# Optimization experiments

Measured on AMD Instinct MI355X. Metric: run time of the kernel, lower is better.

The kernel has to match this reference:

```python
import jax, jax.numpy as jnp
import numpy as np

# Dimensions
NT, NS = 1000, 2048   # timesteps, basins
NF, NG = 6, 32        # forcing channels, static attributes
NH, NR, HS = 16, 8, 256  # buckets, routing taps, hidden size
NK, NGD = 3, 9        # len(kDict)=3 (km,ki,ke), len(gDict)=9


def setup_inputs() -> dict:
    key = jax.random.key(0)
    ks = jax.random.split(key, 16)
    # Physically plausible forcings: Prcp/Evp nonnegative, T1<=T2 (min/max temp)
    Prcp = jax.random.uniform(ks[0], (NT, NS)) * 10.0
    Evp = jax.random.uniform(ks[1], (NT, NS)) * 5.0
    Tm = jax.random.normal(ks[2], (NT, NS)) * 10.0
    T1 = Tm - jax.random.uniform(ks[3], (NT, NS)) * 5.0
    T2 = Tm + jax.random.uniform(ks[4], (NT, NS)) * 5.0
    Rad = jax.random.uniform(ks[5], (NT, NS))
    Hum = jax.random.uniform(ks[6], (NT, NS))
    x = jnp.stack([Prcp, Evp, T1, T2, Rad, Hum], axis=-1)  # [nt, ns, 6]
    xc = jax.random.normal(ks[7], (NS, NG))

    def lin(k, fan_in, fan_out, s=0.05):
        k1, k2 = jax.random.split(k)
        return (jax.random.normal(k1, (fan_in, fan_out)) * s,
                jax.random.normal(k2, (fan_out,)) * s)

    W_fc, b_fc = lin(ks[8], NG, HS)
    W_r, b_r = lin(ks[9], HS, NH * (NR + 1))
    W_g, b_g = lin(ks[10], HS, NH * NGD)
    W_kin, b_kin = lin(ks[11], 4, HS)
    W_kout, b_kout = lin(ks[12], HS, NH * NK)
    return dict(x=x, xc=xc, W_fc=W_fc, b_fc=b_fc, W_r=W_r, b_r=b_r,
                W_g=W_g, b_g=b_g, W_kin=W_kin, b_kin=b_kin,
                W_kout=W_kout, b_kout=b_kout)


def _hardsigmoid(v):
    return jnp.clip(v / 6.0 + 0.5, 0.0, 1.0)


def _forward(x, xc, W_fc, b_fc, W_r, b_r, W_g, b_g, W_kin, b_kin, W_kout, b_kout):
    nt, ns, _ = x.shape
    Prcp, Evp, T1, T2 = x[..., 0], x[..., 1], x[..., 2], x[..., 3]
    f = x[..., 2:]                        # [nt, ns, 4] (T1,T2,Rad,Hum)

    # ---- getParam (eval mode: DropMask is identity) ----
    state = xc @ W_fc + b_fc              # [ns, hs]
    pK = jnp.tanh(f @ W_kin + b_kin + state) @ W_kout + b_kout  # [nt, ns, nh*3]
    hG = jnp.tanh(state)
    pG = hG @ W_g + b_g                   # [ns, nh*9]
    pR = hG @ W_r + b_r                   # [ns, nh*(nr+1)]

    # sepParam(K): km=exp, ki=relu, ke=exp  -> time-varying [nt, ns, nh]
    km = jnp.exp(pK[..., 0 * NH:1 * NH])
    ki = jax.nn.relu(pK[..., 1 * NH:2 * NH])
    ke = jnp.exp(pK[..., 2 * NH:3 * NH])

    # sepParam(G): static [ns, nh]
    g = lambda i: pG[..., i * NH:(i + 1) * NH]
    kp = jax.nn.sigmoid(g(0))
    ks_ = jax.nn.sigmoid(g(1))
    kd = jax.nn.sigmoid(g(2))
    gd = jax.nn.sigmoid(g(3))
    gl = (jax.nn.sigmoid(g(4)) * 10.0) ** 3
    qb = jax.nn.relu(g(5)) / 10.0
    ga = jax.nn.softmax(g(6), axis=-1)    # area weights over buckets
    gi = _hardsigmoid(g(7)) / 2.0
    ge = jax.nn.relu(g(8))

    # onePeakWeight: unimodal routing weights [ns, nh, nr]
    r = pR.reshape(ns, NH, NR + 1)
    s = jax.nn.softmax(r, axis=-1)
    c = jnp.cumsum(s, axis=-1)
    w = jnp.minimum(c, 1.0 - c + s)[..., :NR]
    wr = w / jnp.sum(w, axis=-1, keepdims=True)

    # divideP: snow/liquid split from min/max temperature crossing 0 C
    fl = jnp.clip(T2 / (T2 - T1 + 1e-5), 0.0, 1.0)  # liquid fraction
    Pl = (Prcp * fl)[..., None]           # [nt, ns, 1]
    Ps = (Prcp * (1.0 - fl))[..., None]
    Ev = Evp[..., None]

    # ---- bucket.step recurrence over time (the custom-scan hot loop) ----
    def step(carry, inp):
        Sf, Ss, Sg = carry                # each [ns, nh]
        Ps_t, Pl_t, Ev_t, km_t, ki_t, ke_t = inp
        # snow bucket: accumulate, melt capped by degree-day factor km
        Sf = Sf + Ps_t
        qf = jnp.minimum(Sf, km_t)
        Sf = Sf - qf
        # partition inflow: impervious/direct fraction gi
        inflow = qf + Pl_t
        qd = inflow * gi
        Ss = Ss + inflow * (1.0 - gi)
        # evapotranspiration
        E = jnp.minimum(jnp.maximum(Ss, 0.0), Ev_t * ke_t * ge)
        Ss = Ss - E
        # interflow capped by ki
        qi = jnp.minimum(ki_t, jnp.maximum(Ss, 0.0))
        Ss = Ss - qi
        # quick flow above capacity gl, slow drainage below
        qp = kp * jnp.maximum(Ss - gl, 0.0)
        qsa = ks_ * jnp.clip(Ss, 0.0, gl)
        Ss = Ss - qp - qsa
        # deep/groundwater bucket: fraction gd percolates, linear reservoir kd + baseflow qb
        Sg = Sg + qsa * gd
        qg = kd * Sg + qb
        Sg = Sg * (1.0 - kd)
        q = qp + qsa * (1.0 - gd) + qg + qd + qi
        return (Sf, Ss, Sg), q

    init = (jnp.zeros((ns, NH), x.dtype),
            jnp.zeros((ns, NH), x.dtype),
            jnp.zeros((ns, NH), x.dtype))
    _, Qp = jax.lax.scan(step, init, (Ps, Pl, Ev, km, ki, ke))  # [nt, ns, nh]

    # routing: valid temporal convolution with per-bucket unit hydrograph wr
    Tout = nt - NR + 1
    Q = jnp.zeros((Tout, ns, NH), Qp.dtype)
    for rr in range(NR):  # NR is a small fixed constant
        Q = Q + Qp[NR - 1 - rr: nt - rr] * wr[..., rr]
    yOut = jnp.sum(Q * ga, axis=-1)       # [Tout, ns]
    return yOut


def reference(x, xc, W_fc, b_fc, W_r, b_r, W_g, b_g, W_kin, b_kin, W_kout, b_kout):
    return _forward(x, xc, W_fc, b_fc, W_r, b_r, W_g, b_g, W_kin, b_kin, W_kout, b_kout)
```

## Files before the change

kernel.cpp:

```cpp
#include <hip/hip_runtime.h>
#include <hip/hip_bf16.h>

#define NT   1000
#define NS   2048
#define NH   16
#define NR   8
#define HS   256
#define TOUT 993

typedef __attribute__((ext_vector_type(8))) short short8;
typedef __attribute__((ext_vector_type(4))) float f32x4;

__device__ __forceinline__ ushort f2bf(float f) {
    union { float f; unsigned int u; } v; v.f = f;
    unsigned int u = v.u;
    return (ushort)((u + 0x7fffu + ((u >> 16) & 1u)) >> 16);
}
__device__ __forceinline__ float bf2f(ushort u) {
    union { unsigned int i; float f; } v; v.i = ((unsigned int)u) << 16; return v.f;
}
__device__ __forceinline__ unsigned int packbf2(float lo, float hi) {
    union { __hip_bfloat162 b; unsigned int u; } v;
    v.b = __float22bfloat162_rn(make_float2(lo, hi));
    return v.u;
}
__device__ __forceinline__ float sigf(float x) { return 1.f / (1.f + __expf(-x)); }
__device__ __forceinline__ float fast_tanh(float z) {
    float e = exp2f(z * 2.885390082f);
    return 1.f - 2.f * __builtin_amdgcn_rcpf(e + 1.f);
}
__device__ __forceinline__ float2 f2fma(float s, float2 w, float2 acc) {
    return make_float2(fmaf(s, w.x, acc.x), fmaf(s, w.y, acc.y));
}
template<int CTRL>
__device__ __forceinline__ float dpp_add(float v) {
    int s = __builtin_amdgcn_update_dpp(0, __builtin_bit_cast(int, v), CTRL, 0xf, 0xf, true);
    return v + __builtin_bit_cast(float, s);
}

__global__ __launch_bounds__(256) void kA(
    const float* __restrict__ xc, const float* __restrict__ W_fc, const float* __restrict__ b_fc,
    const float* __restrict__ W_r, const float* __restrict__ b_r,
    const float* __restrict__ W_g, const float* __restrict__ b_g,
    const float* __restrict__ b_kin, const float* __restrict__ W_kout,
    float* __restrict__ stateK, float* __restrict__ params, ushort* __restrict__ Wt_g)
{
    __shared__ float xcs[32];
    __shared__ float hG[256];
    __shared__ float pGR[288];
    const int s = blockIdx.x, tid = threadIdx.x;

    if (tid < 32) xcs[tid] = xc[s * 32 + tid];
    __syncthreads();

    float acc = b_fc[tid];
#pragma unroll 8
    for (int k = 0; k < 32; ++k) acc = fmaf(xcs[k], W_fc[k * 256 + tid], acc);
    stateK[s * 256 + tid] = acc + b_kin[tid];
    hG[tid] = tanhf(acc);
    __syncthreads();

    for (int j = tid; j < 288; j += 256) {
        const float* W = (j < 144) ? W_g : W_r;
        const float* b = (j < 144) ? b_g : b_r;
        int col = (j < 144) ? j : (j - 144);
        float a = b[col];
#pragma unroll 4
        for (int k = 0; k < 256; ++k) a = fmaf(hG[k], W[k * 144 + col], a);
        pGR[j] = a;
    }
    __syncthreads();

    if (tid < 16) {
        const int h = tid;
        float g0 = pGR[h],       g1 = pGR[16 + h],  g2 = pGR[32 + h];
        float g3 = pGR[48 + h],  g4 = pGR[64 + h],  g5 = pGR[80 + h];
        float g6 = pGR[96 + h],  g7 = pGR[112 + h], g8 = pGR[128 + h];
        float kp = sigf(g0), ksg = sigf(g1), kd = sigf(g2), gd = sigf(g3);
        float t4 = sigf(g4) * 10.f; float gl = t4 * t4 * t4;
        float qb = fmaxf(g5, 0.f) * 0.1f;
        float gi = fminf(fmaxf(g7 * (1.f / 6.f) + 0.5f, 0.f), 1.f) * 0.5f;
        float ge = fmaxf(g8, 0.f);
        float m = g6;
        for (int o = 1; o < 16; o <<= 1) m = fmaxf(m, __shfl_xor(m, o));
        float e = __expf(g6 - m), esum = e;
        for (int o = 1; o < 16; o <<= 1) esum += __shfl_xor(esum, o);
        float ga = e / esum;
        float r[9], rm = -1e30f;
#pragma unroll
        for (int i = 0; i < 9; ++i) { r[i] = pGR[144 + h * 9 + i]; rm = fmaxf(rm, r[i]); }
        float er[9], es = 0.f;
#pragma unroll
        for (int i = 0; i < 9; ++i) { er[i] = __expf(r[i] - rm); es += er[i]; }
        float inv_es = 1.f / es, c = 0.f, wsum = 0.f, w[8];
#pragma unroll
        for (int i = 0; i < 8; ++i) {
            float si = er[i] * inv_es; c += si;
            float wi = fminf(c, 1.f - c + si);
            w[i] = wi; wsum += wi;
        }
        const int base = s * 16 + h;
        params[0 * 32768 + base] = kp;       params[1 * 32768 + base] = ksg;
        params[2 * 32768 + base] = kd;       params[3 * 32768 + base] = gd;
        params[4 * 32768 + base] = gl;       params[5 * 32768 + base] = qb;
        params[6 * 32768 + base] = gi;       params[7 * 32768 + base] = 1.f - gi;
        params[8 * 32768 + base] = 1.f - kd; params[9 * 32768 + base] = 1.f - gd;
        params[10 * 32768 + base] = ge;
        float sc = ga / wsum;
#pragma unroll
        for (int i = 0; i < 8; ++i) params[(11 + i) * 32768 + base] = w[i] * sc;
    }

    if (s == 0) {
        for (int i = tid; i < 48 * 256; i += 256) {
            int k = i / 48, col = i - k * 48;
            Wt_g[col * 264 + k] = f2bf(W_kout[i]);
        }
    }
}

__global__ __launch_bounds__(256, 3) void kB(
    const float* __restrict__ x,
    const float* __restrict__ stateK, const float* __restrict__ W_kin, const float* __restrict__ b_kout,
    const ushort* __restrict__ Wt_g, const float* __restrict__ params,
    unsigned int* __restrict__ kmki, ushort* __restrict__ kevA,
    float2* __restrict__ pspl)
{
    __shared__ ushort Wt[48 * 264];
    __shared__ float  stS[16 * 260];
    __shared__ float  wkS[1024];
    __shared__ float  geS[256];
    __shared__ float  evS[4][5][16];
    const int tid = threadIdx.x;
    const int st = blockIdx.x & 127;
    const int tg = blockIdx.x >> 7;
    const int s0 = st << 4;

    for (int i = tid; i < 3168; i += 256)
        ((uint2*)Wt)[i] = ((const uint2*)Wt_g)[i];
#pragma unroll
    for (int i = tid; i < 1024; i += 256) {
        int row = i >> 6, c = (i & 63) << 2;
        *(float4*)(stS + row * 260 + c) = *(const float4*)(stateK + (s0 + row) * 256 + c);
    }
    *(float4*)(wkS + tid * 4) = ((const float4*)W_kin)[tid];
    geS[tid] = params[10 * 32768 + s0 * 16 + tid];
    __syncthreads();

    const int wv = tid >> 6, lane = tid & 63;
    const int mi = lane & 15, quad = lane >> 4;
    const int site = s0 + mi;
    const int t0 = tg * 20 + wv * 5;

    float xf[5][4];
#pragma unroll
    for (int ti = 0; ti < 5; ++ti) {
        const int t = t0 + ti;
        const int xb = (t * 2048 + site) * 6;
        float2 u23 = *(const float2*)(x + xb + 2);
        float2 u45 = *(const float2*)(x + xb + 4);
        xf[ti][0] = u23.x; xf[ti][1] = u23.y; xf[ti][2] = u45.x; xf[ti][3] = u45.y;
        if (lane < 16) {
            float2 u01 = *(const float2*)(x + xb);
            float fl = fminf(fmaxf(u23.y * __builtin_amdgcn_rcpf(u23.y - u23.x + 1e-5f), 0.f), 1.f);
            const int sg = st * 4 + (mi >> 2), sl = mi & 3;
            pspl[(sg * 1000 + t) * 4 + sl] = make_float2(u01.x * (1.f - fl), u01.x * fl);
            evS[wv][ti][mi] = u01.y;
        }
    }

    const float* stp = stS + mi * 260 + quad * 8;
    const float* wkp = wkS + quad * 8;
    const ushort* Wt0 = Wt + mi * 264 + quad * 8;

    f32x4 acc[5][3];
#pragma unroll
    for (int ti = 0; ti < 5; ++ti)
#pragma unroll
        for (int j = 0; j < 3; ++j) acc[ti][j] = (f32x4){0.f, 0.f, 0.f, 0.f};

#pragma unroll 1
    for (int kk = 0; kk < 8; ++kk) {
        const int ko = kk * 32;
        float4 sa  = *(const float4*)(stp + ko);
        float4 sb  = *(const float4*)(stp + ko + 4);
        float4 w0a = *(const float4*)(wkp + ko);
        float4 w0b = *(const float4*)(wkp + ko + 4);
        float4 w1a = *(const float4*)(wkp + 256 + ko);
        float4 w1b = *(const float4*)(wkp + 256 + ko + 4);
        float4 w2a = *(const float4*)(wkp + 512 + ko);
        float4 w2b = *(const float4*)(wkp + 512 + ko + 4);
        float4 w3a = *(const float4*)(wkp + 768 + ko);
        float4 w3b = *(const float4*)(wkp + 768 + ko + 4);
        short8 b0 = *(const short8*)(Wt0 + ko);
        short8 b1 = *(const short8*)(Wt0 + 16 * 264 + ko);
        short8 b2 = *(const short8*)(Wt0 + 32 * 264 + ko);
#pragma unroll
        for (int ti = 0; ti < 5; ++ti) {
            const float x0 = xf[ti][0], x1 = xf[ti][1], x2 = xf[ti][2], x3 = xf[ti][3];
            float2 z0 = make_float2(sa.x, sa.y), z1 = make_float2(sa.z, sa.w);
            float2 z2 = make_float2(sb.x, sb.y), z3 = make_float2(sb.z, sb.w);
            z0 = f2fma(x0, make_float2(w0a.x, w0a.y), z0);
            z1 = f2fma(x0, make_float2(w0a.z, w0a.w), z1);
            z2 = f2fma(x0, make_float2(w0b.x, w0b.y), z2);
            z3 = f2fma(x0, make_float2(w0b.z, w0b.w), z3);
            z0 = f2fma(x1, make_float2(w1a.x, w1a.y), z0);
            z1 = f2fma(x1, make_float2(w1a.z, w1a.w), z1);
            z2 = f2fma(x1, make_float2(w1b.x, w1b.y), z2);
            z3 = f2fma(x1, make_float2(w1b.z, w1b.w), z3);
            z0 = f2fma(x2, make_float2(w2a.x, w2a.y), z0);
            z1 = f2fma(x2, make_float2(w2a.z, w2a.w), z1);
            z2 = f2fma(x2, make_float2(w2b.x, w2b.y), z2);
            z3 = f2fma(x2, make_float2(w2b.z, w2b.w), z3);
            z0 = f2fma(x3, make_float2(w3a.x, w3a.y), z0);
            z1 = f2fma(x3, make_float2(w3a.z, w3a.w), z1);
            z2 = f2fma(x3, make_float2(w3b.x, w3b.y), z2);
            z3 = f2fma(x3, make_float2(w3b.z, w3b.w), z3);
            union { short8 s; unsigned int u[4]; } a;
            a.u[0] = packbf2(fast_tanh(z0.x), fast_tanh(z0.y));
            a.u[1] = packbf2(fast_tanh(z1.x), fast_tanh(z1.y));
            a.u[2] = packbf2(fast_tanh(z2.x), fast_tanh(z2.y));
            a.u[3] = packbf2(fast_tanh(z3.x), fast_tanh(z3.y));
            acc[ti][0] = __builtin_amdgcn_mfma_f32_16x16x32_bf16(a.s, b0, acc[ti][0], 0, 0, 0);
            acc[ti][1] = __builtin_amdgcn_mfma_f32_16x16x32_bf16(a.s, b1, acc[ti][1], 0, 0, 0);
            acc[ti][2] = __builtin_amdgcn_mfma_f32_16x16x32_bf16(a.s, b2, acc[ti][2], 0, 0, 0);
        }
    }

    const float bo0 = b_kout[mi], bo1 = b_kout[16 + mi], bo2 = b_kout[32 + mi];
    const int sgW = st * 4 + quad;
#pragma unroll
    for (int ti = 0; ti < 5; ++ti) {
        const int t = t0 + ti;
#pragma unroll
        for (int reg = 0; reg < 4; ++reg) {
            const int sl = quad * 4 + reg;
            float km = __expf(acc[ti][0][reg] + bo0);
            float ki = fmaxf(acc[ti][1][reg] + bo1, 0.f);
            float ke = __expf(acc[ti][2][reg] + bo2);
            float kev = ke * evS[wv][ti][sl] * geS[sl * 16 + mi];
            const int idx = (sgW * 1000 + t) * 64 + (reg << 4) + mi;
            kmki[idx] = (unsigned int)f2bf(km) | ((unsigned int)f2bf(ki) << 16);
            kevA[idx] = f2bf(kev);
        }
    }
}

__global__ __launch_bounds__(64, 1) void kC(
    const unsigned int* __restrict__ kmki, const ushort* __restrict__ kevA,
    const float2* __restrict__ pspl,
    const float* __restrict__ params, float* __restrict__ yOut)
{
    const int tid = threadIdx.x;
    const int sg = blockIdx.x;
    const int sl = tid >> 4;
    const int s = sg * 4 + sl;
    const int h = tid & 15;
    const int gid = s * 16 + h;

    const float kp  = params[0 * 32768 + gid];
    const float ks_ = params[1 * 32768 + gid];
    const float kd  = params[2 * 32768 + gid];
    const float gd  = params[3 * 32768 + gid];
    const float gl  = params[4 * 32768 + gid];
    const float qbv = params[5 * 32768 + gid];
    const float gi  = params[6 * 32768 + gid];
    const float gi1 = params[7 * 32768 + gid];
    const float kd1 = params[8 * 32768 + gid];
    const float gd1 = params[9 * 32768 + gid];
    float wrga[8];
#pragma unroll
    for (int i = 0; i < 8; ++i) wrga[i] = params[(11 + i) * 32768 + gid];

    float Sf = 0.f, Ss = 0.f, Sg = 0.f;
    float qh[8];
#pragma unroll
    for (int i = 0; i < 8; ++i) qh[i] = 0.f;

    const int base = sg * 1000;

    unsigned int a0[8], a1[8], a2[8]; ushort e0[8], e1[8], e2[8];
    float2 p0[8], p1[8], p2[8];

#define LOADB(B, tb) do {                                               \
        const int _b = base + (tb) * 8;                                 \
        _Pragma("unroll")                                               \
        for (int i = 0; i < 8; ++i) {                                   \
            a##B[i] = kmki[(_b + i) * 64 + tid];                        \
            e##B[i] = kevA[(_b + i) * 64 + tid];                        \
            p##B[i] = pspl[(_b + i) * 4 + sl];                          \
        }                                                               \
    } while (0)

#define COMPUTEB(B, tb) do {                                            \
        float z[8];                                                     \
        _Pragma("unroll")                                               \
        for (int i = 0; i < 8; ++i) {                                   \
            float km = __builtin_bit_cast(float, a##B[i] << 16);        \
            float ki = __builtin_bit_cast(float, a##B[i] & 0xffff0000u);\
            float kev = __builtin_bit_cast(float, ((unsigned int)e##B[i]) << 16); \
            float ps = p##B[i].x, pl = p##B[i].y;                       \
            Sf += ps;                                                   \
            float qf = fminf(Sf, km); Sf -= qf;                         \
            float inflow = qf + pl;                                     \
            float qd = inflow * gi;                                     \
            Ss = fmaf(inflow, gi1, Ss);                                 \
            float E = fminf(Ss, kev); Ss -= E;                          \
            float qi = fminf(ki, Ss); Ss -= qi;                         \
            float qp = kp * fmaxf(Ss - gl, 0.f);                        \
            float qsa = ks_ * fminf(Ss, gl);                            \
            Ss -= qp + qsa;                                             \
            Sg = fmaf(qsa, gd, Sg);                                     \
            float qg = fmaf(kd, Sg, qbv);                               \
            Sg *= kd1;                                                  \
            float q = fmaf(qsa, gd1, qp) + qg + qd + qi;                \
            qh[i] = q;                                                  \
            float v = 0.f;                                              \
            _Pragma("unroll")                                           \
            for (int k = 0; k < 8; ++k) v = fmaf(wrga[k], qh[(i - k) & 7], v); \
            z[i] = v;                                                   \
        }                                                               \
        _Pragma("unroll")                                               \
        for (int i = 0; i < 8; ++i) z[i] = dpp_add<0xB1>(z[i]);         \
        _Pragma("unroll")                                               \
        for (int i = 0; i < 8; ++i) z[i] = dpp_add<0x4E>(z[i]);         \
        _Pragma("unroll")                                               \
        for (int i = 0; i < 8; ++i) z[i] = dpp_add<0x141>(z[i]);        \
        _Pragma("unroll")                                               \
        for (int i = 0; i < 8; ++i) z[i] = dpp_add<0x140>(z[i]);        \
        if (h == 0) {                                                   \
            const int tbase = (tb) * 8;                                 \
            _Pragma("unroll")                                           \
            for (int i = 0; i < 8; ++i) {                               \
                const int t = tbase + i;                                \
                if (t >= 7) yOut[(t - 7) * 2048 + s] = z[i];            \
            }                                                           \
        }                                                               \
    } while (0)

    LOADB(0, 0);
    LOADB(1, 1);
    LOADB(2, 2);

    for (int it = 0; it < 42; ++it) {
        const int tb = it * 3;
        COMPUTEB(0, tb);
        LOADB(0, (tb + 3 <= 124) ? tb + 3 : 124);
        if (tb + 1 < 125) {
            COMPUTEB(1, tb + 1);
            LOADB(1, (tb + 4 <= 124) ? tb + 4 : 124);
        }
        if (tb + 2 < 125) {
            COMPUTEB(2, tb + 2);
            LOADB(2, (tb + 5 <= 124) ? tb + 5 : 124);
        }
    }
#undef LOADB
#undef COMPUTEB
}

extern "C" void kernel_launch(void* const* d_in, const int* in_sizes, int n_in,
                              void* d_out, int out_size, void* d_ws, size_t ws_size,
                              hipStream_t stream) {
    const float* x      = (const float*)d_in[0];
    const float* xc     = (const float*)d_in[1];
    const float* W_fc   = (const float*)d_in[2];
    const float* b_fc   = (const float*)d_in[3];
    const float* W_r    = (const float*)d_in[4];
    const float* b_r    = (const float*)d_in[5];
    const float* W_g    = (const float*)d_in[6];
    const float* b_g    = (const float*)d_in[7];
    const float* W_kin  = (const float*)d_in[8];
    const float* b_kin  = (const float*)d_in[9];
    const float* W_kout = (const float*)d_in[10];
    const float* b_kout = (const float*)d_in[11];
    float* yOut = (float*)d_out;

    char* ws = (char*)d_ws;
    float*  stateK = (float*)(ws + 0);
    float*  params = (float*)(ws + (2 << 20));
    ushort* Wt_g   = (ushort*)(ws + (6 << 20));
    char*   p      = ws + (6 << 20) + (128 << 10);
    float2* pspl   = (float2*)p;
    unsigned int* kmki = (unsigned int*)(p + 16384000);
    ushort* kevA   = (ushort*)(p + 16384000 + 131072000);

    hipLaunchKernelGGL(kA, dim3(2048), dim3(256), 0, stream,
                       xc, W_fc, b_fc, W_r, b_r, W_g, b_g, b_kin, W_kout,
                       stateK, params, Wt_g);
    hipLaunchKernelGGL(kB, dim3(128 * 50), dim3(256), 0, stream,
                       x, stateK, W_kin, b_kout, Wt_g, params, kmki, kevA, pspl);
    hipLaunchKernelGGL(kC, dim3(512), dim3(64), 0, stream,
                       kmki, kevA, pspl, params, yOut);
}
```

Before: 560.9 us.

## Compute first-layer f@W_kin+state with split-bf16 MFMA instead of scalar FMAs

The small K=4 first-layer projection in kB moves from packed scalar FMAs onto MFMA. W_kin and the forcings are each split into bf16 hi/lo parts so the hi*hi, hi*lo and lo*hi terms keep near-fp32 accuracy, and the state row is used as the accumulator input. W_kout is re-permuted in kA so the MFMA output layout of the hidden activations matches the B operand of the second MFMA. This removes about 16 VALU FMAs per 8 hidden units per timestep, at the cost of two extra MFMAs, operand masking and a small drop in precision.

```diff
diff --git a/kernel.cpp b/kernel.cpp
--- a/kernel.cpp
+++ b/kernel.cpp
@@ -29,9 +29,6 @@
     float e = exp2f(z * 2.885390082f);
     return 1.f - 2.f * __builtin_amdgcn_rcpf(e + 1.f);
 }
-__device__ __forceinline__ float2 f2fma(float s, float2 w, float2 acc) {
-    return make_float2(fmaf(s, w.x, acc.x), fmaf(s, w.y, acc.y));
-}
 template<int CTRL>
 __device__ __forceinline__ float dpp_add(float v) {
     int s = __builtin_amdgcn_update_dpp(0, __builtin_bit_cast(int, v), CTRL, 0xf, 0xf, true);
@@ -42,8 +39,10 @@
     const float* __restrict__ xc, const float* __restrict__ W_fc, const float* __restrict__ b_fc,
     const float* __restrict__ W_r, const float* __restrict__ b_r,
     const float* __restrict__ W_g, const float* __restrict__ b_g,
-    const float* __restrict__ b_kin, const float* __restrict__ W_kout,
-    float* __restrict__ stateK, float* __restrict__ params, ushort* __restrict__ Wt_g)
+    const float* __restrict__ W_kin, const float* __restrict__ b_kin,
+    const float* __restrict__ W_kout,
+    float* __restrict__ stateK, float* __restrict__ params,
+    ushort* __restrict__ Wt_g, ushort* __restrict__ whlo_g)
 {
     __shared__ float xcs[32];
     __shared__ float hG[256];
@@ -113,22 +112,36 @@
 
     if (s == 0) {
         for (int i = tid; i < 48 * 256; i += 256) {
-            int k = i / 48, col = i - k * 48;
-            Wt_g[col * 264 + k] = f2bf(W_kout[i]);
+            int col = i % 48, slot = i / 48;
+            int kk = slot >> 5, q = (slot >> 3) & 3, j = slot & 7;
+            int h = kk * 32 + ((j < 4) ? (q * 4 + j) : (16 + q * 4 + (j - 4)));
+            Wt_g[col * 264 + slot] = f2bf(W_kout[h * 48 + col]);
+        }
+        {
+            const int h = tid;
+#pragma unroll
+            for (int f = 0; f < 4; ++f) {
+                float w = W_kin[f * 256 + h];
+                ushort hi = f2bf(w);
+                float lo = w - bf2f(hi);
+                whlo_g[h * 8 + f] = hi;
+                whlo_g[h * 8 + 4 + f] = f2bf(lo);
+            }
         }
     }
 }
 
 __global__ __launch_bounds__(256, 3) void kB(
     const float* __restrict__ x,
-    const float* __restrict__ stateK, const float* __restrict__ W_kin, const float* __restrict__ b_kout,
-    const ushort* __restrict__ Wt_g, const float* __restrict__ params,
+    const float* __restrict__ stateK, const float* __restrict__ b_kout,
+    const ushort* __restrict__ Wt_g, const ushort* __restrict__ whlo_g,
+    const float* __restrict__ params,
     unsigned int* __restrict__ kmki, ushort* __restrict__ kevA,
     float2* __restrict__ pspl)
 {
     __shared__ ushort Wt[48 * 264];
     __shared__ float  stS[16 * 260];
-    __shared__ float  wkS[1024];
+    __shared__ ushort whloS[2048];
     __shared__ float  geS[256];
     __shared__ float  evS[4][5][16];
     const int tid = threadIdx.x;
@@ -143,7 +156,7 @@
         int row = i >> 6, c = (i & 63) << 2;
         *(float4*)(stS + row * 260 + c) = *(const float4*)(stateK + (s0 + row) * 256 + c);
     }
-    *(float4*)(wkS + tid * 4) = ((const float4*)W_kin)[tid];
+    *(float4*)(whloS + tid * 8) = ((const float4*)whlo_g)[tid];
     geS[tid] = params[10 * 32768 + s0 * 16 + tid];
     __syncthreads();
 
@@ -169,9 +182,25 @@
         }
     }
 
-    const float* stp = stS + mi * 260 + quad * 8;
-    const float* wkp = wkS + quad * 8;
+    unsigned int bfr[5][4];
+#pragma unroll
+    for (int ti = 0; ti < 5; ++ti) {
+        const float x0 = xf[ti][0], x1 = xf[ti][1], x2 = xf[ti][2], x3 = xf[ti][3];
+        unsigned int h01 = packbf2(x0, x1), h23 = packbf2(x2, x3);
+        float l0 = x0 - bf2f((ushort)(h01 & 0xffffu));
+        float l1 = x1 - bf2f((ushort)(h01 >> 16));
+        float l2 = x2 - bf2f((ushort)(h23 & 0xffffu));
+        float l3 = x3 - bf2f((ushort)(h23 >> 16));
+        unsigned int l01 = packbf2(l0, l1), l23 = packbf2(l2, l3);
+        bfr[ti][0] = (quad == 0) ? h01 : (quad == 1 ? l01 : 0u);
+        bfr[ti][1] = (quad == 0) ? h23 : (quad == 1 ? l23 : 0u);
+        bfr[ti][2] = (quad == 0) ? h01 : 0u;
+        bfr[ti][3] = (quad == 0) ? h23 : 0u;
+    }
+
+    const float*  stp = stS + mi * 260;
     const ushort* Wt0 = Wt + mi * 264 + quad * 8;
+    const int q4 = quad * 4;
 
     f32x4 acc[5][3];
 #pragma unroll
@@ -182,45 +211,38 @@
 #pragma unroll 1
     for (int kk = 0; kk < 8; ++kk) {
         const int ko = kk * 32;
-        float4 sa  = *(const float4*)(stp + ko);
-        float4 sb  = *(const float4*)(stp + ko + 4);
-        float4 w0a = *(const float4*)(wkp + ko);
-        float4 w0b = *(const float4*)(wkp + ko + 4);
-        float4 w1a = *(const float4*)(wkp + 256 + ko);
-        float4 w1b = *(const float4*)(wkp + 256 + ko + 4);
-        float4 w2a = *(const float4*)(wkp + 512 + ko);
-        float4 w2b = *(const float4*)(wkp + 512 + ko + 4);
-        float4 w3a = *(const float4*)(wkp + 768 + ko);
-        float4 w3b = *(const float4*)(wkp + 768 + ko + 4);
+        union { short8 s; unsigned int u[4]; } W0, W1, A0, A1;
+        W0.s = *(const short8*)(whloS + (ko + mi) * 8);
+        W1.s = *(const short8*)(whloS + (ko + 16 + mi) * 8);
+        A0.u[0] = (quad <= 1) ? W0.u[0] : 0u;
+        A0.u[1] = (quad <= 1) ? W0.u[1] : 0u;
+        A0.u[2] = (quad == 0) ? W0.u[2] : 0u;
+        A0.u[3] = (quad == 0) ? W0.u[3] : 0u;
+        A1.u[0] = (quad <= 1) ? W1.u[0] : 0u;
+        A1.u[1] = (quad <= 1) ? W1.u[1] : 0u;
+        A1.u[2] = (quad == 0) ? W1.u[2] : 0u;
+        A1.u[3] = (quad == 0) ? W1.u[3] : 0u;
+        f32x4 c0 = *(const f32x4*)(stp + ko + q4);
+        f32x4 c1 = *(const f32x4*)(stp + ko + 16 + q4);
         short8 b0 = *(const short8*)(Wt0 + ko);
         short8 b1 = *(const short8*)(Wt0 + 16 * 264 + ko);
         short8 b2 = *(const short8*)(Wt0 + 32 * 264 + ko);
 #pragma unroll
         for (int ti = 0; ti < 5; ++ti) {
-            const float x0 = xf[ti][0], x1 = xf[ti][1], x2 = xf[ti][2], x3 = xf[ti][3];
-            float2 z0 = make_float2(sa.x, sa.y), z1 = make_float2(sa.z, sa.w);
-            float2 z2 = make_float2(sb.x, sb.y), z3 = make_float2(sb.z, sb.w);
-            z0 = f2fma(x0, make_float2(w0a.x, w0a.y), z0);
-            z1 = f2fma(x0, make_float2(w0a.z, w0a.w), z1);
-            z2 = f2fma(x0, make_float2(w0b.x, w0b.y), z2);
-            z3 = f2fma(x0, make_float2(w0b.z, w0b.w), z3);
-            z0 = f2fma(x1, make_float2(w1a.x, w1a.y), z0);
-            z1 = f2fma(x1, make_float2(w1a.z, w1a.w), z1);
-            z2 = f2fma(x1, make_float2(w1b.x, w1b.y), z2);
-            z3 = f2fma(x1, make_float2(w1b.z, w1b.w), z3);
-            z0 = f2fma(x2, make_float2(w2a.x, w2a.y), z0);
-            z1 = f2fma(x2, make_float2(w2a.z, w2a.w), z1);
-            z2 = f2fma(x2, make_float2(w2b.x, w2b.y), z2);
-            z3 = f2fma(x2, make_float2(w2b.z, w2b.w), z3);
-            z0 = f2fma(x3, make_float2(w3a.x, w3a.y), z0);
-            z1 = f2fma(x3, make_float2(w3a.z, w3a.w), z1);
-            z2 = f2fma(x3, make_float2(w3b.x, w3b.y), z2);
-            z3 = f2fma(x3, make_float2(w3b.z, w3b.w), z3);
+            union { short8 s; unsigned int u[4]; } B;
+            B.u[0] = bfr[ti][0]; B.u[1] = bfr[ti][1];
+            B.u[2] = bfr[ti][2]; B.u[3] = bfr[ti][3];
+            f32x4 z0 = __builtin_amdgcn_mfma_f32_16x16x32_bf16(A0.s, B.s, c0, 0, 0, 0);
+            f32x4 z1 = __builtin_amdgcn_mfma_f32_16x16x32_bf16(A1.s, B.s, c1, 0, 0, 0);
+            float t0_ = fast_tanh(z0[0]), t1_ = fast_tanh(z0[1]);
+            float t2_ = fast_tanh(z0[2]), t3_ = fast_tanh(z0[3]);
+            float t4_ = fast_tanh(z1[0]), t5_ = fast_tanh(z1[1]);
+            float t6_ = fast_tanh(z1[2]), t7_ = fast_tanh(z1[3]);
             union { short8 s; unsigned int u[4]; } a;
-            a.u[0] = packbf2(fast_tanh(z0.x), fast_tanh(z0.y));
-            a.u[1] = packbf2(fast_tanh(z1.x), fast_tanh(z1.y));
-            a.u[2] = packbf2(fast_tanh(z2.x), fast_tanh(z2.y));
-            a.u[3] = packbf2(fast_tanh(z3.x), fast_tanh(z3.y));
+            a.u[0] = packbf2(t0_, t1_);
+            a.u[1] = packbf2(t2_, t3_);
+            a.u[2] = packbf2(t4_, t5_);
+            a.u[3] = packbf2(t6_, t7_);
             acc[ti][0] = __builtin_amdgcn_mfma_f32_16x16x32_bf16(a.s, b0, acc[ti][0], 0, 0, 0);
             acc[ti][1] = __builtin_amdgcn_mfma_f32_16x16x32_bf16(a.s, b1, acc[ti][1], 0, 0, 0);
             acc[ti][2] = __builtin_amdgcn_mfma_f32_16x16x32_bf16(a.s, b2, acc[ti][2], 0, 0, 0);
@@ -380,16 +402,17 @@
     float*  stateK = (float*)(ws + 0);
     float*  params = (float*)(ws + (2 << 20));
     ushort* Wt_g   = (ushort*)(ws + (6 << 20));
+    ushort* whlo_g = (ushort*)(ws + (6 << 20) + (64 << 10));
     char*   p      = ws + (6 << 20) + (128 << 10);
     float2* pspl   = (float2*)p;
     unsigned int* kmki = (unsigned int*)(p + 16384000);
     ushort* kevA   = (ushort*)(p + 16384000 + 131072000);
 
     hipLaunchKernelGGL(kA, dim3(2048), dim3(256), 0, stream,
-                       xc, W_fc, b_fc, W_r, b_r, W_g, b_g, b_kin, W_kout,
-                       stateK, params, Wt_g);
+                       xc, W_fc, b_fc, W_r, b_r, W_g, b_g, W_kin, b_kin, W_kout,
+                       stateK, params, Wt_g, whlo_g);
     hipLaunchKernelGGL(kB, dim3(128 * 50), dim3(256), 0, stream,
-                       x, stateK, W_kin, b_kout, Wt_g, params, kmki, kevA, pspl);
+                       x, stateK, b_kout, Wt_g, whlo_g, params, kmki, kevA, pspl);
     hipLaunchKernelGGL(kC, dim3(512), dim3(64), 0, stream,
                        kmki, kevA, pspl, params, yOut);
 }
```

Measured after the change: 533.0 us. -5.0%, faster.
